# Kernel optimization log

Measured on AMD Instinct MI355X. Metric: run time of the kernel, lower is better.

Reference implementation:

```python
import jax, jax.numpy as jnp
import numpy as np

FIX_SIGMA = (1.0, 2.0, 4.0, 8.0, 16.0)


def setup_inputs() -> dict:
    key = jax.random.key(0)
    k1, k2 = jax.random.split(key)
    B, C, D = 512, 32, 512
    source = jax.random.normal(k1, (B, C, D), dtype=jnp.float32)
    target = jax.random.normal(k2, (B, C, D), dtype=jnp.float32)
    return {"source": source, "target": target}


def _mmd(source, target):
    B = source.shape[0]
    total = jnp.concatenate([source, target], axis=0)  # [N, C, D], N = 2B
    # Pairwise per-channel squared L2 distance via norm expansion
    # (mathematically identical to ((x_i - x_j)**2).sum(-1), no [N,N,C,D] intermediate)
    sq = jnp.sum(total * total, axis=-1)  # [N, C]
    cross = jnp.einsum("icd,jcd->ijc", total, total)  # [N, N, C]
    L2 = sq[:, None, :] + sq[None, :, :] - 2.0 * cross  # [N, N, C]
    kernels = sum(jnp.exp(-L2 / sigma) for sigma in FIX_SIGMA)  # [N, N, C]
    XX = kernels[:B, :B, :]
    YY = kernels[B:, B:, :]
    XY = kernels[:B, B:, :]
    YX = kernels[B:, :B, :]
    loss_1 = XX + YY - XY - YX  # [B, B, C]
    # mean over dim0, mean over dim0 again (i.e. both batch dims), sum over channels
    return jnp.sum(jnp.mean(loss_1, axis=(0, 1)))


def reference(source, target):
    return _mmd(source, target)
```

## Files before the change

### kernel.cpp

```cpp
#include <hip/hip_runtime.h>

namespace {

constexpr int kC = 32;
constexpr int kD = 512;
constexpr int kB = 512;
constexpr int kN = 1024;
constexpr int kCD = kC * kD;
constexpr int BM = 128;
constexpr int KT = kD / 32;
constexpr int TILES = kN / BM;
constexpr int NP = TILES * (TILES + 1) / 2;

typedef float f32x4 __attribute__((ext_vector_type(4)));

__device__ inline unsigned int f32_to_e4m3(float x) {
  unsigned int u = __float_as_uint(x);
  unsigned int s = (u >> 24) & 0x80u;
  unsigned int ax = u & 0x7fffffffu;
  if (ax < 0x3c800000u) {
    unsigned int m = (unsigned int)(__uint_as_float(ax) * 512.0f + 0.5f);
    return s | (m > 7u ? 8u : m);
  }
  if (ax > 0x43e00000u) return s | 0x7eu;
  unsigned int r = ax + 0x7ffffu + ((ax >> 20) & 1u);
  unsigned int e = (r >> 23) - 120u;
  return s | (e << 3) | ((r >> 20) & 7u);
}

__global__ void prep_kernel(const float* __restrict__ src,
                            const float* __restrict__ tgt,
                            float* __restrict__ sq,
                            unsigned char* __restrict__ tot,
                            float* __restrict__ out) {
  if (blockIdx.x == 0 && threadIdx.x == 0) *out = 0.f;
  const int seg = blockIdx.x >> 5;
  const int c = blockIdx.x & 31;
  const int t = threadIdx.x;
  const int slot = t & 15;
  const int ks = t >> 4;

  const int i = seg * 16 + slot;
  const float* p = (i < kB ? src + (size_t)i * kCD
                           : tgt + (size_t)(i - kB) * kCD) + c * kD + ks * 32;

  __shared__ unsigned int stg[2048];
  __shared__ float sqp[256];

  float part = 0.f;
#pragma unroll
  for (int q = 0; q < 4; ++q) {
    f32x4 v0 = *(const f32x4*)(p + q * 8);
    f32x4 v1 = *(const f32x4*)(p + q * 8 + 4);
    part += v0.x * v0.x + v0.y * v0.y + v0.z * v0.z + v0.w * v0.w
          + v1.x * v1.x + v1.y * v1.y + v1.z * v1.z + v1.w * v1.w;
    unsigned int lo = f32_to_e4m3(v0.x) | (f32_to_e4m3(v0.y) << 8) |
                      (f32_to_e4m3(v0.z) << 16) | (f32_to_e4m3(v0.w) << 24);
    unsigned int hi = f32_to_e4m3(v1.x) | (f32_to_e4m3(v1.y) << 8) |
                      (f32_to_e4m3(v1.z) << 16) | (f32_to_e4m3(v1.w) << 24);
    int idx = ks * 128 + q * 32 + slot * 2;
    stg[idx] = lo;
    stg[idx + 1] = hi;
  }
  sqp[t] = part;
  __syncthreads();

  unsigned char* gout = tot + (size_t)(c * 64 + seg) * 8192;
  ((uint4*)gout)[t * 2]     = ((const uint4*)stg)[t * 2];
  ((uint4*)gout)[t * 2 + 1] = ((const uint4*)stg)[t * 2 + 1];

  if (t < 16) {
    float s = 0.f;
#pragma unroll
    for (int j = 0; j < 16; ++j) s += sqp[t + 16 * j];
    sq[c * kN + seg * 16 + t] = s;
  }
}

__launch_bounds__(256, 4)
__global__ void mmd_kernel(const unsigned char* __restrict__ tot,
                           const float* __restrict__ sq,
                           float* __restrict__ out) {
  const int b = blockIdx.x;
  const int c = b & 31;
  int p = b >> 5;
  int ti = 0;
  while (p >= TILES - ti) { p -= TILES - ti; ++ti; }
  const int tj = ti + p;

  __shared__ __align__(16) unsigned char lA[3][4096];
  __shared__ __align__(16) unsigned char lB[3][4096];
  __shared__ float wsum[4];

  const int t = threadIdx.x;
  const int lane = t & 63;
  const int wid = t >> 6;
  const int wr = wid >> 1;
  const int wcn = wid & 1;

  const size_t blkA = (size_t)(c * 64 + ti * 8 + 2 * wid + (lane >> 5));
  const size_t blkB = (size_t)(c * 64 + tj * 8 + 2 * wid + (lane >> 5));
  const int loff16 = (lane & 31) * 16;

  auto STAGE = [&](int buf, int ks) {
    const unsigned char* sa = tot + (blkA * 16 + ks) * 512 + loff16;
    const unsigned char* sb = tot + (blkB * 16 + ks) * 512 + loff16;
    __builtin_amdgcn_global_load_lds(
        (const __attribute__((address_space(1))) unsigned int*)sa,
        (__attribute__((address_space(3))) unsigned int*)&lA[buf][wid * 1024],
        16, 0, 0);
    __builtin_amdgcn_global_load_lds(
        (const __attribute__((address_space(1))) unsigned int*)sb,
        (__attribute__((address_space(3))) unsigned int*)&lB[buf][wid * 1024],
        16, 0, 0);
  };

  const int fo = ((lane >> 4) << 4) + (lane & 15);

  f32x4 acc[4][4] = {};

  STAGE(0, 0);
  STAGE(1, 1);

#pragma unroll
  for (int ks = 0; ks < KT; ++ks) {
    if (ks + 1 < KT) asm volatile("s_waitcnt vmcnt(2)" ::: "memory");
    else             asm volatile("s_waitcnt vmcnt(0)" ::: "memory");
    __builtin_amdgcn_sched_barrier(0);
    __builtin_amdgcn_s_barrier();

    const int buf = ks % 3;
    const long* A64 = (const long*)lA[buf];
    const long* B64 = (const long*)lB[buf];
    long aF[4], bF[4];
#pragma unroll
    for (int m = 0; m < 4; ++m) aF[m] = A64[(4 * wr + m) * 64 + fo];
#pragma unroll
    for (int n = 0; n < 4; ++n) bF[n] = B64[(4 * wcn + n) * 64 + fo];

    if (ks + 2 < KT) STAGE((ks + 2) % 3, ks + 2);

    __builtin_amdgcn_s_setprio(1);
#pragma unroll
    for (int m = 0; m < 4; ++m)
#pragma unroll
      for (int n = 0; n < 4; ++n)
        acc[m][n] = __builtin_amdgcn_mfma_f32_16x16x32_fp8_fp8(
            aF[m], bF[n], acc[m][n], 0, 0, 0);
    __builtin_amdgcn_s_setprio(0);
  }

  const float sgn = ((ti < TILES / 2) == (tj < TILES / 2)) ? 1.f : -1.f;
  const bool diag = (ti == tj);
  const float scale = sgn * (diag ? 1.f : 2.f) / 262144.f;
  const float* sqA = sq + c * kN + ti * BM + wr * 64;
  const float* sqB = sq + c * kN + tj * BM + wcn * 64;
  const int s4 = lane >> 4, l15 = lane & 15;

  float local = 0.f;
#pragma unroll
  for (int m = 0; m < 4; ++m) {
    float sqa_r[4];
#pragma unroll
    for (int rI = 0; rI < 4; ++rI)
      sqa_r[rI] = sqA[m * 16 + s4 * 4 + rI];
#pragma unroll
    for (int n = 0; n < 4; ++n) {
      float sqb_ = sqB[n * 16 + l15];
#pragma unroll
      for (int rI = 0; rI < 4; ++rI) {
        float L2 = sqa_r[rI] + sqb_ - 2.f * acc[m][n][rI];
        if (diag && (wr * 64 + m * 16 + s4 * 4 + rI) ==
                    (wcn * 64 + n * 16 + l15))
          L2 = 0.f;
        float tt = __expf(L2 * -0.0625f);
        float t2 = tt * tt, t4 = t2 * t2, t8 = t4 * t4;
        local += tt + t2 + t4 + t8 + t8 * t8;
      }
    }
  }
  local *= scale;

#pragma unroll
  for (int o = 32; o > 0; o >>= 1) local += __shfl_down(local, o);
  if (lane == 0) wsum[wid] = local;
  __syncthreads();
  if (t == 0)
    atomicAdd(out, wsum[0] + wsum[1] + wsum[2] + wsum[3]);
}

}

extern "C" void kernel_launch(void* const* d_in, const int* in_sizes, int n_in,
                              void* d_out, int out_size, void* d_ws,
                              size_t ws_size, hipStream_t stream) {
  const float* src = (const float*)d_in[0];
  const float* tgt = (const float*)d_in[1];
  float* out = (float*)d_out;

  float* sq = (float*)d_ws;
  unsigned char* tot = (unsigned char*)d_ws + (size_t)kC * kN * 4;

  {
    int blocks = 64 * kC;
    prep_kernel<<<blocks, 256, 0, stream>>>(src, tgt, sq, tot, out);
  }
  {
    int blocks = NP * kC;
    mmd_kernel<<<blocks, 256, 0, stream>>>(tot, sq, out);
  }
}
```

Baseline: 62.13 us.

## Double-buffer 64-wide K stages in MMD GEMM and coalesce prep loads

The MMD kernel now stages two 32-wide K chunks per iteration into a double buffer, replacing the triple buffer of single chunks. This halves the number of barrier and wait rounds, and each round runs 32 MFMAs per wave. The loads for the next stage are issued right after the barrier, but each iteration waits for vmcnt(0), so there is less lookahead than with the previous two-deep prefetch. The prep kernel remaps threads so the 16 consecutive threads in a group read contiguous 32-float chunks of one row, which should coalesce global reads better. The squared-norm reduction indexing is adjusted to match.

After: 61.21 us. Within noise of the previous version (-1.5%).

```diff
diff --git a/kernel.cpp b/kernel.cpp
--- a/kernel.cpp
+++ b/kernel.cpp
@@ -8,7 +8,7 @@
 constexpr int kN = 1024;
 constexpr int kCD = kC * kD;
 constexpr int BM = 128;
-constexpr int KT = kD / 32;
+constexpr int KT2 = kD / 64;
 constexpr int TILES = kN / BM;
 constexpr int NP = TILES * (TILES + 1) / 2;
 
@@ -37,8 +37,8 @@
   const int seg = blockIdx.x >> 5;
   const int c = blockIdx.x & 31;
   const int t = threadIdx.x;
-  const int slot = t & 15;
-  const int ks = t >> 4;
+  const int slot = t >> 4;
+  const int ks = t & 15;
 
   const int i = seg * 16 + slot;
   const float* p = (i < kB ? src + (size_t)i * kCD
@@ -72,7 +72,7 @@
   if (t < 16) {
     float s = 0.f;
 #pragma unroll
-    for (int j = 0; j < 16; ++j) s += sqp[t + 16 * j];
+    for (int j = 0; j < 16; ++j) s += sqp[t * 16 + j];
     sq[c * kN + seg * 16 + t] = s;
   }
 }
@@ -88,8 +88,8 @@
   while (p >= TILES - ti) { p -= TILES - ti; ++ti; }
   const int tj = ti + p;
 
-  __shared__ __align__(16) unsigned char lA[3][4096];
-  __shared__ __align__(16) unsigned char lB[3][4096];
+  __shared__ __align__(16) unsigned char lA[2][8192];
+  __shared__ __align__(16) unsigned char lB[2][8192];
   __shared__ float wsum[4];
 
   const int t = threadIdx.x;
@@ -98,21 +98,26 @@
   const int wr = wid >> 1;
   const int wcn = wid & 1;
 
-  const size_t blkA = (size_t)(c * 64 + ti * 8 + 2 * wid + (lane >> 5));
-  const size_t blkB = (size_t)(c * 64 + tj * 8 + 2 * wid + (lane >> 5));
-  const int loff16 = (lane & 31) * 16;
-
-  auto STAGE = [&](int buf, int ks) {
-    const unsigned char* sa = tot + (blkA * 16 + ks) * 512 + loff16;
-    const unsigned char* sb = tot + (blkB * 16 + ks) * 512 + loff16;
-    __builtin_amdgcn_global_load_lds(
-        (const __attribute__((address_space(1))) unsigned int*)sa,
-        (__attribute__((address_space(3))) unsigned int*)&lA[buf][wid * 1024],
-        16, 0, 0);
-    __builtin_amdgcn_global_load_lds(
-        (const __attribute__((address_space(1))) unsigned int*)sb,
-        (__attribute__((address_space(3))) unsigned int*)&lB[buf][wid * 1024],
-        16, 0, 0);
+  const int blkA0 = c * 64 + ti * 8;
+  const int blkB0 = c * 64 + tj * 8;
+
+  auto STAGE = [&](int buf, int kt) {
+#pragma unroll
+    for (int q = 0; q < 2; ++q) {
+      int seg = wid * 2 + q;
+      const unsigned char* sa =
+          tot + ((size_t)(blkA0 + seg) * 16 + 2 * kt) * 512 + lane * 16;
+      const unsigned char* sb =
+          tot + ((size_t)(blkB0 + seg) * 16 + 2 * kt) * 512 + lane * 16;
+      __builtin_amdgcn_global_load_lds(
+          (const __attribute__((address_space(1))) unsigned int*)sa,
+          (__attribute__((address_space(3))) unsigned int*)&lA[buf][seg * 1024],
+          16, 0, 0);
+      __builtin_amdgcn_global_load_lds(
+          (const __attribute__((address_space(1))) unsigned int*)sb,
+          (__attribute__((address_space(3))) unsigned int*)&lB[buf][seg * 1024],
+          16, 0, 0);
+    }
   };
 
   const int fo = ((lane >> 4) << 4) + (lane & 15);
@@ -120,33 +125,38 @@
   f32x4 acc[4][4] = {};
 
   STAGE(0, 0);
-  STAGE(1, 1);
-
-#pragma unroll
-  for (int ks = 0; ks < KT; ++ks) {
-    if (ks + 1 < KT) asm volatile("s_waitcnt vmcnt(2)" ::: "memory");
-    else             asm volatile("s_waitcnt vmcnt(0)" ::: "memory");
+
+#pragma unroll
+  for (int kt = 0; kt < KT2; ++kt) {
+    asm volatile("s_waitcnt vmcnt(0)" ::: "memory");
     __builtin_amdgcn_sched_barrier(0);
     __builtin_amdgcn_s_barrier();
 
-    const int buf = ks % 3;
+    const int buf = kt & 1;
+    if (kt + 1 < KT2) STAGE(buf ^ 1, kt + 1);
+
     const long* A64 = (const long*)lA[buf];
     const long* B64 = (const long*)lB[buf];
-    long aF[4], bF[4];
-#pragma unroll
-    for (int m = 0; m < 4; ++m) aF[m] = A64[(4 * wr + m) * 64 + fo];
-#pragma unroll
-    for (int n = 0; n < 4; ++n) bF[n] = B64[(4 * wcn + n) * 64 + fo];
-
-    if (ks + 2 < KT) STAGE((ks + 2) % 3, ks + 2);
+    long aF[2][4], bF[2][4];
+#pragma unroll
+    for (int pi = 0; pi < 2; ++pi) {
+#pragma unroll
+      for (int m = 0; m < 4; ++m)
+        aF[pi][m] = A64[(4 * wr + m) * 128 + pi * 64 + fo];
+#pragma unroll
+      for (int n = 0; n < 4; ++n)
+        bF[pi][n] = B64[(4 * wcn + n) * 128 + pi * 64 + fo];
+    }
 
     __builtin_amdgcn_s_setprio(1);
 #pragma unroll
-    for (int m = 0; m < 4; ++m)
-#pragma unroll
-      for (int n = 0; n < 4; ++n)
-        acc[m][n] = __builtin_amdgcn_mfma_f32_16x16x32_fp8_fp8(
-            aF[m], bF[n], acc[m][n], 0, 0, 0);
+    for (int pi = 0; pi < 2; ++pi)
+#pragma unroll
+      for (int m = 0; m < 4; ++m)
+#pragma unroll
+        for (int n = 0; n < 4; ++n)
+          acc[m][n] = __builtin_amdgcn_mfma_f32_16x16x32_fp8_fp8(
+              aF[pi][m], bF[pi][n], acc[m][n], 0, 0, 0);
     __builtin_amdgcn_s_setprio(0);
   }
 
```
